# Performance work log

Hardware: AMD Instinct MI355X
Metric: run time of the kernel (lower is better)

Reference implementation:

```python
import jax, jax.numpy as jnp
import numpy as np

EPS = 1e-5  # GroupNorm eps


def setup_inputs() -> dict:
    key = jax.random.key(0)
    ks = jax.random.split(key, 12)
    D, H, I = 512, 8, 64
    B, L = 2, 1024
    g = 0.01  # xavier gain used in reset_parameters
    inp = {
        "x": jax.random.normal(ks[0], (B, L, D), jnp.float32),
        "w_z": jax.random.normal(ks[1], (D, D), jnp.float32) * g,
        "b_z": jnp.zeros((D,), jnp.float32),
        "w_za": jax.random.normal(ks[2], (D, D), jnp.float32) * g,
        "b_za": jnp.zeros((D,), jnp.float32),
        "w_ang": jax.random.normal(ks[3], (D, H), jnp.float32) * g,
        "b_ang": jnp.zeros((H,), jnp.float32),
        "w_abs": jax.random.normal(ks[4], (D, H), jnp.float32) * g,
        "b_abs": jnp.zeros((H,), jnp.float32),
        "w_y": jax.random.normal(ks[5], (D, D), jnp.float32) * g,
        "b_y": jnp.zeros((D,), jnp.float32),
        "w_ya": jax.random.normal(ks[6], (D, D), jnp.float32) * g,
        "b_ya": jnp.zeros((D,), jnp.float32),
        "gn_w": jnp.ones((H,), jnp.float32),
        "gn_b": jnp.zeros((H,), jnp.float32),
        "lc_r": jax.random.normal(ks[7], (H, I), jnp.float32),
        "lc_i": jax.random.normal(ks[8], (H, I), jnp.float32),
    }
    return inp


def reference(x, w_z, b_z, w_za, b_za, w_ang, b_ang, w_abs, b_abs,
              w_y, b_y, w_ya, b_ya, gn_w, gn_b, lc_r, lc_i):
    B, L, D = x.shape
    H = gn_w.shape[0]
    I = D // H
    silu = jax.nn.silu
    xf = x.astype(jnp.float32)

    # gated value, promoted to complex:  [B, L, H, I]
    z = ((xf @ w_z + b_z) * silu(xf @ w_za + b_za)).astype(jnp.complex64).reshape(B, L, H, I)

    # per-head log-decay phazor: [B, L, H] complex
    scale = (0.001 ** jnp.linspace(0.0, 1.0, H)).astype(jnp.float32)
    ln_ph = (silu(xf @ w_ang + b_ang) * 1j - jax.nn.sigmoid(xf @ w_abs + b_abs)) * scale

    # FFT of ones => circular conv with ones = cumulative sum along axis 1
    ones_fft = jnp.fft.fft(jnp.ones((L,), jnp.float32), n=2 * L)

    # ln_phazor repeated over m then tril(-1) over the LAST TWO dims (m, h),
    # exactly matching torch.Tensor.tril semantics on a 'b l m h' tensor.
    masked = jnp.tril(jnp.broadcast_to(ln_ph[:, :, None, :], (B, L, L, H)), -1)
    mfft = jnp.fft.fft(masked, n=2 * L, axis=1)
    mconv = jnp.fft.ifft(mfft * ones_fft[None, :, None, None], axis=1)[:, :L]
    ph_masked = jnp.tril(jnp.exp(mconv))  # tril over (m, h)

    h_inner = jnp.einsum('blmh,bmhi->blhi', ph_masked, z)

    pfft = jnp.fft.fft(ln_ph, n=2 * L, axis=1)
    pconv = jnp.fft.ifft(pfft * ones_fft[None, :, None], axis=1)[:, :L]
    last_conv = lc_r + 1j * lc_i  # [H, I] complex (last_conv_init broadcast over batch)
    h_cross = jnp.exp(pconv)[..., None] * last_conv[None, None]  # [B, L, H, I]

    h = (h_inner + h_cross).real  # [B, L, H, I]

    # GroupNorm(H groups, H channels) on (B*L, H, I): per-(sample, head) norm over I
    mean = h.mean(axis=-1, keepdims=True)
    var = h.var(axis=-1, keepdims=True)
    hn = (h - mean) / jnp.sqrt(var + EPS) * gn_w[:, None] + gn_b[:, None]
    h_norm = hn.reshape(B, L, D)

    y = (h_norm @ w_y + b_y) * silu(xf @ w_ya + b_ya)
    return y.astype(x.dtype)
```

## Files before the change

kernel.cpp:

```cpp
#include <hip/hip_runtime.h>
#include <math.h>

#define D_ 512
#define H_ 8
#define I_ 64
#define L_ 1024

typedef __attribute__((ext_vector_type(8))) short short8;
typedef __attribute__((ext_vector_type(4))) float f32x4;

__device__ __forceinline__ float sigmoidf_(float x) { return 1.f / (1.f + expf(-x)); }
__device__ __forceinline__ float siluf_(float x) { return x / (1.f + expf(-x)); }

__device__ __forceinline__ unsigned short f2bf(float f) {
    unsigned u = __float_as_uint(f);
    u += 0x7fffu + ((u >> 16) & 1u);
    return (unsigned short)(u >> 16);
}
__device__ __forceinline__ float bf2f(unsigned short v) {
    return __uint_as_float((unsigned)v << 16);
}

__global__ __launch_bounds__(256) void k1_prep(
    const float* __restrict__ x, unsigned short* __restrict__ xb, int nconv,
    const float* __restrict__ w0, const float* __restrict__ w1,
    const float* __restrict__ w2, const float* __restrict__ w3,
    unsigned short* __restrict__ t0, unsigned short* __restrict__ t1,
    unsigned short* __restrict__ t2, unsigned short* __restrict__ t3,
    const float* __restrict__ w_ang, const float* __restrict__ b_ang,
    const float* __restrict__ w_abs, const float* __restrict__ b_abs,
    float* __restrict__ a_out, float* __restrict__ r_out)
{
    __shared__ float sm[64][65];
    const int tid = threadIdx.x;
    const int bid = blockIdx.x;
    if (bid < nconv) {
        int gid = bid * 256 + tid;
        float4 v = ((const float4*)x)[gid];
        ushort4 o = { f2bf(v.x), f2bf(v.y), f2bf(v.z), f2bf(v.w) };
        ((ushort4*)xb)[gid] = o;
        return;
    }
    if (bid < nconv + 256) {
        int t = bid - nconv;
        int zsel = t >> 6, tile = t & 63;
        const float* src = zsel == 0 ? w0 : zsel == 1 ? w1 : zsel == 2 ? w2 : w3;
        unsigned short* dst = zsel == 0 ? t0 : zsel == 1 ? t1 : zsel == 2 ? t2 : t3;
        const int k0 = (tile >> 3) * 64, n0 = (tile & 7) * 64;
#pragma unroll
        for (int i = 0; i < 16; ++i) {
            int idx = tid + i * 256;
            int rr = idx >> 6, cc = idx & 63;
            sm[rr][cc] = src[(size_t)(k0 + rr) * 512 + n0 + cc];
        }
        __syncthreads();
#pragma unroll
        for (int i = 0; i < 16; ++i) {
            int idx = tid + i * 256;
            int rr = idx >> 6, cc = idx & 63;
            dst[(size_t)(n0 + rr) * 512 + k0 + cc] = f2bf(sm[cc][rr]);
        }
        return;
    }
    {
        int t = bid - nconv - 256;
        const int s = tid & 3, c = (tid >> 2) & 15, r = tid >> 6;
        const int n = t * 4 + r;
        const int h = c & 7;
        const float* wp = (c < 8) ? w_ang : w_abs;
        const float* xr = x + (size_t)n * D_;
        float acc = 0.f;
#pragma unroll 4
        for (int i = 0; i < 128; ++i) {
            int k = i * 4 + s;
            acc = fmaf(xr[k], wp[k * H_ + h], acc);
        }
        acc += __shfl_xor(acc, 1);
        acc += __shfl_xor(acc, 2);
        if (s == 0) {
            const float scale = expf(-6.9077552789821368f * (h * (1.0f / 7.0f)));
            if (c < 8) { float p = acc + b_ang[h]; a_out[(size_t)n * H_ + h] = siluf_(p) * scale; }
            else       { float p = acc + b_abs[h]; r_out[(size_t)n * H_ + h] = sigmoidf_(p) * scale; }
        }
    }
}

__global__ __launch_bounds__(256) void k2_gemm3_scan(
    const unsigned short* __restrict__ Axb,
    const unsigned short* __restrict__ Wz, const unsigned short* __restrict__ Wza,
    const unsigned short* __restrict__ Wya,
    const float* __restrict__ b_z, const float* __restrict__ b_za, const float* __restrict__ b_ya,
    unsigned short* __restrict__ gateb, float* __restrict__ Zs_part, float* __restrict__ zdiag,
    const float* __restrict__ a_arr, const float* __restrict__ r_arr,
    float* __restrict__ Si, float* __restrict__ Sr, int nby)
{
    __shared__ short As[64 * 32];
    __shared__ short Bs[3][64 * 32];
    __shared__ float red[64][8];
    __shared__ float2 buf[2][256];
    const int tid = threadIdx.x;

    if ((int)blockIdx.y >= nby) {
        const int u = ((int)blockIdx.y - nby) * 8 + (int)blockIdx.x;
        const int b = u >> 3, h = u & 7;
        float2 v[4];
        float2 run = make_float2(0.f, 0.f);
        const size_t base = ((size_t)b * L_ + tid * 4) * H_ + h;
#pragma unroll
        for (int j = 0; j < 4; ++j) {
            run.x += a_arr[base + j * H_];
            run.y += r_arr[base + j * H_];
            v[j] = run;
        }
        buf[0][tid] = run;
        __syncthreads();
        int src = 0;
        for (int off = 1; off < 256; off <<= 1) {
            float2 val = buf[src][tid];
            if (tid >= off) { float2 p = buf[src][tid - off]; val.x += p.x; val.y += p.y; }
            buf[src ^ 1][tid] = val;
            src ^= 1;
            __syncthreads();
        }
        float2 excl = make_float2(0.f, 0.f);
        if (tid > 0) excl = buf[src][tid - 1];
#pragma unroll
        for (int j = 0; j < 4; ++j) {
            Si[base + j * H_] = v[j].x + excl.x;
            Sr[base + j * H_] = -(v[j].y + excl.y);
        }
        return;
    }

    const int lane = tid & 63, w = tid >> 6;
    const int wm = w >> 1, wn = w & 1;
    const int bx = blockIdx.x;
    const int row0 = blockIdx.y * 64, col0 = bx * 64;

    const f32x4 zf = {0.f, 0.f, 0.f, 0.f};
    f32x4 accz[2][2], accza[2][2], accya[2][2];
#pragma unroll
    for (int a = 0; a < 2; ++a)
#pragma unroll
        for (int bq = 0; bq < 2; ++bq) { accz[a][bq] = zf; accza[a][bq] = zf; accya[a][bq] = zf; }

    const int sr = tid >> 2, sc = tid & 3;
    const int sld = sr * 64 + ((sc ^ ((sr >> 1) & 3)) << 4);
    const size_t gA = (size_t)(row0 + sr) * 512 + sc * 8;
    const size_t gB = (size_t)(col0 + sr) * 512 + sc * 8;

    for (int k0 = 0; k0 < 512; k0 += 32) {
        *(int4*)((char*)As + sld)    = *(const int4*)(Axb + gA + k0);
        *(int4*)((char*)Bs[0] + sld) = *(const int4*)(Wz  + gB + k0);
        *(int4*)((char*)Bs[1] + sld) = *(const int4*)(Wza + gB + k0);
        *(int4*)((char*)Bs[2] + sld) = *(const int4*)(Wya + gB + k0);
        __syncthreads();
        short8 af[2], bz[2], bza[2], bya[2];
#pragma unroll
        for (int fi = 0; fi < 2; ++fi) {
            int rr = wm * 32 + fi * 16 + (lane & 15);
            int off = rr * 64 + ((((lane >> 4)) ^ ((rr >> 1) & 3)) << 4);
            af[fi] = *(const short8*)((const char*)As + off);
        }
#pragma unroll
        for (int fj = 0; fj < 2; ++fj) {
            int rr = wn * 32 + fj * 16 + (lane & 15);
            int off = rr * 64 + ((((lane >> 4)) ^ ((rr >> 1) & 3)) << 4);
            bz[fj]  = *(const short8*)((const char*)Bs[0] + off);
            bza[fj] = *(const short8*)((const char*)Bs[1] + off);
            bya[fj] = *(const short8*)((const char*)Bs[2] + off);
        }
#pragma unroll
        for (int fi = 0; fi < 2; ++fi)
#pragma unroll
            for (int fj = 0; fj < 2; ++fj) {
                accz[fi][fj]  = __builtin_amdgcn_mfma_f32_16x16x32_bf16(af[fi], bz[fj],  accz[fi][fj],  0, 0, 0);
                accza[fi][fj] = __builtin_amdgcn_mfma_f32_16x16x32_bf16(af[fi], bza[fj], accza[fi][fj], 0, 0, 0);
                accya[fi][fj] = __builtin_amdgcn_mfma_f32_16x16x32_bf16(af[fi], bya[fj], accya[fi][fj], 0, 0, 0);
            }
        __syncthreads();
    }

    const bool first = (row0 & (L_ - 1)) == 0;
    const int b8 = (row0 >> 10) * 8;
#pragma unroll
    for (int fj = 0; fj < 2; ++fj) {
        float lsum = 0.f;
        int lc = wn * 32 + fj * 16 + (lane & 15);
        int col = col0 + lc;
        float Bz = b_z[col], Bza = b_za[col], Bya = b_ya[col];
#pragma unroll
        for (int fi = 0; fi < 2; ++fi) {
#pragma unroll
            for (int q = 0; q < 4; ++q) {
                int lr = wm * 32 + fi * 16 + ((lane >> 4) << 2) + q;
                int row = row0 + lr;
                float pz = accz[fi][fj][q] + Bz;
                float pza = accza[fi][fj][q] + Bza;
                float v = pz * siluf_(pza);
                gateb[(size_t)row * 512 + col] = f2bf(siluf_(accya[fi][fj][q] + Bya));
                if (!first || lr > bx) lsum += v;
                if (first && lr == bx) zdiag[(b8 + bx) * 64 + lc] = v;
            }
        }
        red[lc][wm * 4 + (lane >> 4)] = lsum;
    }
    __syncthreads();
    if (tid < 64) {
        float s = 0.f;
#pragma unroll
        for (int j = 0; j < 8; ++j) s += red[tid][j];
        Zs_part[((size_t)blockIdx.y * 8 + bx) * 64 + tid] = s;
    }
}

__global__ __launch_bounds__(512) void k3_hgn_gemm_y(
    const unsigned short* __restrict__ Wy, const float* __restrict__ b_y,
    const unsigned short* __restrict__ gateb,
    const float* __restrict__ Sr, const float* __restrict__ Si,
    const float* __restrict__ Zs_part, const float* __restrict__ zdiag,
    const float* __restrict__ lc_r, const float* __restrict__ lc_i,
    const float* __restrict__ gn_w, const float* __restrict__ gn_b,
    float* __restrict__ y)
{
    __shared__ unsigned short hA[64][520];
    __shared__ short Bs[64 * 32];
    __shared__ float Cr[8][65], Ci[8][65], Zd[8][65];
    const int tid = threadIdx.x;
    const int row0 = blockIdx.y * 64, col0 = blockIdx.x * 64;
    const int b = row0 >> 10;

    {
        int h = tid >> 6, i = tid & 63;
        float s = 0.f;
#pragma unroll
        for (int rb = 0; rb < 16; ++rb)
            s += Zs_part[(((size_t)b * 16 + rb) * 8 + h) * 64 + i];
        Cr[h][i] = s + lc_r[h * 64 + i];
        Ci[h][i] = lc_i[h * 64 + i];
        Zd[h][i] = zdiag[((size_t)b * 8 + h) * 64 + i];
    }
    __syncthreads();

    {
        const int r = tid >> 3, h = tid & 7;
        const int row = row0 + r;
        const float sr = Sr[(size_t)row * 8 + h];
        const float si = Si[(size_t)row * 8 + h];
        const float er = expf(sr);
        const float ca = er * cosf(si), sb = er * sinf(si);
        float sum = 0.f, sq = 0.f;
#pragma unroll 8
        for (int i = 0; i < 64; ++i) {
            float hv = Zd[h][i] + ca * Cr[h][i] - sb * Ci[h][i];
            sum += hv; sq += hv * hv;
        }
        const float mean = sum * (1.f / 64.f);
        const float inv = rsqrtf(sq * (1.f / 64.f) - mean * mean + 1e-5f);
        const float gw = gn_w[h] * inv;
        const float gb = gn_b[h] - mean * gw;
#pragma unroll
        for (int s8 = 0; s8 < 8; ++s8) {
            short8 pk;
#pragma unroll
            for (int j = 0; j < 8; ++j) {
                int i = s8 * 8 + j;
                float hv = Zd[h][i] + ca * Cr[h][i] - sb * Ci[h][i];
                pk[j] = (short)f2bf(hv * gw + gb);
            }
            int slot = (s8 + h) & 7;
            *(short8*)((char*)&hA[r][0] + h * 128 + slot * 16) = pk;
        }
    }
    __syncthreads();

    const int lane = tid & 63, w = tid >> 6;
    const int wm = w >> 2, wn = w & 3;
    const f32x4 zf = {0.f, 0.f, 0.f, 0.f};
    f32x4 acc[2] = {zf, zf};

    const int brow = tid >> 3, bsc = tid & 7;
    const size_t gB = (size_t)(col0 + brow) * 512 + bsc * 4;
    const int bwr = brow * 64 + (((bsc >> 1) ^ ((brow >> 1) & 3)) << 4) + (bsc & 1) * 8;

    for (int k0 = 0; k0 < 512; k0 += 32) {
        *(int2*)((char*)Bs + bwr) = *(const int2*)(Wy + gB + k0);
        __syncthreads();
        short8 af[2], bf;
        const int hk = k0 >> 6;
        const int t = ((k0 & 32) >> 3) + (lane >> 4);
        const int slot = (t + hk) & 7;
#pragma unroll
        for (int fi = 0; fi < 2; ++fi) {
            int rr = wm * 32 + fi * 16 + (lane & 15);
            af[fi] = *(const short8*)((const char*)&hA[rr][0] + hk * 128 + slot * 16);
        }
        {
            int rr = wn * 16 + (lane & 15);
            bf = *(const short8*)((const char*)Bs + rr * 64 + (((lane >> 4) ^ ((rr >> 1) & 3)) << 4));
        }
        acc[0] = __builtin_amdgcn_mfma_f32_16x16x32_bf16(af[0], bf, acc[0], 0, 0, 0);
        acc[1] = __builtin_amdgcn_mfma_f32_16x16x32_bf16(af[1], bf, acc[1], 0, 0, 0);
        __syncthreads();
    }

    const int col = col0 + wn * 16 + (lane & 15);
    const float By = b_y[col];
#pragma unroll
    for (int fi = 0; fi < 2; ++fi)
#pragma unroll
        for (int q = 0; q < 4; ++q) {
            int row = row0 + wm * 32 + fi * 16 + ((lane >> 4) << 2) + q;
            size_t idx = (size_t)row * 512 + col;
            y[idx] = (acc[fi][q] + By) * bf2f(gateb[idx]);
        }
}

extern "C" void kernel_launch(void* const* d_in, const int* in_sizes, int n_in,
                              void* d_out, int out_size, void* d_ws, size_t ws_size,
                              hipStream_t stream) {
    (void)n_in; (void)out_size; (void)ws_size;
    const float* x     = (const float*)d_in[0];
    const float* w_z   = (const float*)d_in[1];
    const float* b_z   = (const float*)d_in[2];
    const float* w_za  = (const float*)d_in[3];
    const float* b_za  = (const float*)d_in[4];
    const float* w_ang = (const float*)d_in[5];
    const float* b_ang = (const float*)d_in[6];
    const float* w_abs = (const float*)d_in[7];
    const float* b_abs = (const float*)d_in[8];
    const float* w_y   = (const float*)d_in[9];
    const float* b_y   = (const float*)d_in[10];
    const float* w_ya  = (const float*)d_in[11];
    const float* b_ya  = (const float*)d_in[12];
    const float* gn_w  = (const float*)d_in[13];
    const float* gn_b  = (const float*)d_in[14];
    const float* lc_r  = (const float*)d_in[15];
    const float* lc_i  = (const float*)d_in[16];
    float* y = (float*)d_out;

    const int BL = in_sizes[0] / D_;
    const int B  = BL / L_;

    unsigned short* xb   = (unsigned short*)d_ws;
    unsigned short* wtz  = xb   + (size_t)BL * 512;
    unsigned short* wtza = wtz  + 512 * 512;
    unsigned short* wtya = wtza + 512 * 512;
    unsigned short* wty  = wtya + 512 * 512;
    unsigned short* gateb= wty  + 512 * 512;
    float* a_arr = (float*)(gateb + (size_t)BL * 512);
    float* r_arr = a_arr + (size_t)BL * H_;
    float* Si    = r_arr + (size_t)BL * H_;
    float* Sr    = Si    + (size_t)BL * H_;
    float* zdiag = Sr    + (size_t)BL * H_;
    float* Zs_part = zdiag + (size_t)B * H_ * I_;

    const int nconv = (BL * 512) / 1024;
    const int nby = BL / 64;

    k1_prep<<<nconv + 256 + BL / 4, 256, 0, stream>>>(
        x, xb, nconv, w_z, w_za, w_ya, w_y, wtz, wtza, wtya, wty,
        w_ang, b_ang, w_abs, b_abs, a_arr, r_arr);
    k2_gemm3_scan<<<dim3(8, nby + 2), 256, 0, stream>>>(
        xb, wtz, wtza, wtya, b_z, b_za, b_ya,
        gateb, Zs_part, zdiag, a_arr, r_arr, Si, Sr, nby);
    k3_hgn_gemm_y<<<dim3(8, nby), 512, 0, stream>>>(
        wty, b_y, gateb, Sr, Si, Zs_part, zdiag, lc_r, lc_i, gn_w, gn_b, y);
}
```

Baseline: 47.24 us.

## Double-buffer GEMM tiles via global_load_lds and fuse decay projections into scan blocks

```diff
diff --git a/kernel.cpp b/kernel.cpp
--- a/kernel.cpp
+++ b/kernel.cpp
@@ -19,6 +19,11 @@
 }
 __device__ __forceinline__ float bf2f(unsigned short v) {
     return __uint_as_float((unsigned)v << 16);
+}
+
+__device__ __forceinline__ void load_lds16(const void* g, void* l) {
+    __builtin_amdgcn_global_load_lds((const __attribute__((address_space(1))) void*)g,
+                                     (__attribute__((address_space(3))) void*)l, 16, 0, 0);
 }
 
 __global__ __launch_bounds__(256) void k1_prep(
@@ -27,9 +32,8 @@
     const float* __restrict__ w2, const float* __restrict__ w3,
     unsigned short* __restrict__ t0, unsigned short* __restrict__ t1,
     unsigned short* __restrict__ t2, unsigned short* __restrict__ t3,
-    const float* __restrict__ w_ang, const float* __restrict__ b_ang,
-    const float* __restrict__ w_abs, const float* __restrict__ b_abs,
-    float* __restrict__ a_out, float* __restrict__ r_out)
+    const float* __restrict__ w_ang, const float* __restrict__ w_abs,
+    float* __restrict__ wat, float* __restrict__ wrt)
 {
     __shared__ float sm[64][65];
     const int tid = threadIdx.x;
@@ -63,24 +67,10 @@
         return;
     }
     {
-        int t = bid - nconv - 256;
-        const int s = tid & 3, c = (tid >> 2) & 15, r = tid >> 6;
-        const int n = t * 4 + r;
-        const int h = c & 7;
-        const float* wp = (c < 8) ? w_ang : w_abs;
-        const float* xr = x + (size_t)n * D_;
-        float acc = 0.f;
-#pragma unroll 4
-        for (int i = 0; i < 128; ++i) {
-            int k = i * 4 + s;
-            acc = fmaf(xr[k], wp[k * H_ + h], acc);
-        }
-        acc += __shfl_xor(acc, 1);
-        acc += __shfl_xor(acc, 2);
-        if (s == 0) {
-            const float scale = expf(-6.9077552789821368f * (h * (1.0f / 7.0f)));
-            if (c < 8) { float p = acc + b_ang[h]; a_out[(size_t)n * H_ + h] = siluf_(p) * scale; }
-            else       { float p = acc + b_abs[h]; r_out[(size_t)n * H_ + h] = sigmoidf_(p) * scale; }
+        int h = bid - nconv - 256;
+        for (int k = tid; k < 512; k += 256) {
+            wat[h * 512 + k] = w_ang[k * 8 + h];
+            wrt[h * 512 + k] = w_abs[k * 8 + h];
         }
     }
 }
@@ -91,25 +81,39 @@
     const unsigned short* __restrict__ Wya,
     const float* __restrict__ b_z, const float* __restrict__ b_za, const float* __restrict__ b_ya,
     unsigned short* __restrict__ gateb, float* __restrict__ Zs_part, float* __restrict__ zdiag,
-    const float* __restrict__ a_arr, const float* __restrict__ r_arr,
-    float* __restrict__ Si, float* __restrict__ Sr, int nby)
+    const float* __restrict__ x, const float* __restrict__ wat, const float* __restrict__ wrt,
+    const float* __restrict__ b_ang, const float* __restrict__ b_abs,
+    float* __restrict__ Si, float* __restrict__ Sr)
 {
-    __shared__ short As[64 * 32];
-    __shared__ short Bs[3][64 * 32];
+    __shared__ short As[2][2048];
+    __shared__ short Bs[2][3][2048];
     __shared__ float red[64][8];
     __shared__ float2 buf[2][256];
     const int tid = threadIdx.x;
 
-    if ((int)blockIdx.y >= nby) {
-        const int u = ((int)blockIdx.y - nby) * 8 + (int)blockIdx.x;
-        const int b = u >> 3, h = u & 7;
+    if ((int)blockIdx.y < 2) {
+        const int b = blockIdx.y, h = blockIdx.x;
+        const float scale = expf(-6.9077552789821368f * (h * (1.0f / 7.0f)));
+        const float ba = b_ang[h], br = b_abs[h];
+        const float4* wa4 = (const float4*)(wat + h * 512);
+        const float4* wr4 = (const float4*)(wrt + h * 512);
         float2 v[4];
         float2 run = make_float2(0.f, 0.f);
-        const size_t base = ((size_t)b * L_ + tid * 4) * H_ + h;
+        const float* xp = x + ((size_t)b * L_ + tid * 4) * 512;
 #pragma unroll
         for (int j = 0; j < 4; ++j) {
-            run.x += a_arr[base + j * H_];
-            run.y += r_arr[base + j * H_];
+            const float4* xr = (const float4*)(xp + (size_t)j * 512);
+            float aA = 0.f, aR = 0.f;
+#pragma unroll 8
+            for (int q = 0; q < 128; ++q) {
+                float4 xv = xr[q], wa = wa4[q], wr = wr4[q];
+                aA = fmaf(xv.x, wa.x, aA); aA = fmaf(xv.y, wa.y, aA);
+                aA = fmaf(xv.z, wa.z, aA); aA = fmaf(xv.w, wa.w, aA);
+                aR = fmaf(xv.x, wr.x, aR); aR = fmaf(xv.y, wr.y, aR);
+                aR = fmaf(xv.z, wr.z, aR); aR = fmaf(xv.w, wr.w, aR);
+            }
+            run.x += siluf_(aA + ba) * scale;
+            run.y += sigmoidf_(aR + br) * scale;
             v[j] = run;
         }
         buf[0][tid] = run;
@@ -124,6 +128,7 @@
         }
         float2 excl = make_float2(0.f, 0.f);
         if (tid > 0) excl = buf[src][tid - 1];
+        const size_t base = ((size_t)b * L_ + tid * 4) * H_ + h;
 #pragma unroll
         for (int j = 0; j < 4; ++j) {
             Si[base + j * H_] = v[j].x + excl.x;
@@ -135,7 +140,8 @@
     const int lane = tid & 63, w = tid >> 6;
     const int wm = w >> 1, wn = w & 1;
     const int bx = blockIdx.x;
-    const int row0 = blockIdx.y * 64, col0 = bx * 64;
+    const int rblk = (int)blockIdx.y - 2;
+    const int row0 = rblk * 64, col0 = bx * 64;
 
     const f32x4 zf = {0.f, 0.f, 0.f, 0.f};
     f32x4 accz[2][2], accza[2][2], accya[2][2];
@@ -144,31 +150,41 @@
 #pragma unroll
         for (int bq = 0; bq < 2; ++bq) { accz[a][bq] = zf; accza[a][bq] = zf; accya[a][bq] = zf; }
 
-    const int sr = tid >> 2, sc = tid & 3;
-    const int sld = sr * 64 + ((sc ^ ((sr >> 1) & 3)) << 4);
-    const size_t gA = (size_t)(row0 + sr) * 512 + sc * 8;
-    const size_t gB = (size_t)(col0 + sr) * 512 + sc * 8;
-
-    for (int k0 = 0; k0 < 512; k0 += 32) {
-        *(int4*)((char*)As + sld)    = *(const int4*)(Axb + gA + k0);
-        *(int4*)((char*)Bs[0] + sld) = *(const int4*)(Wz  + gB + k0);
-        *(int4*)((char*)Bs[1] + sld) = *(const int4*)(Wza + gB + k0);
-        *(int4*)((char*)Bs[2] + sld) = *(const int4*)(Wya + gB + k0);
-        __syncthreads();
+    const int ssr = w * 16 + (lane >> 2);
+    const int ssc = (lane & 3) ^ ((ssr >> 1) & 3);
+    const size_t gA = (size_t)(row0 + ssr) * 512 + ssc * 8;
+    const size_t gB = (size_t)(col0 + ssr) * 512 + ssc * 8;
+    const int ldso = w * 1024;
+
+    load_lds16(Axb + gA, (char*)As[0] + ldso);
+    load_lds16(Wz  + gB, (char*)Bs[0][0] + ldso);
+    load_lds16(Wza + gB, (char*)Bs[0][1] + ldso);
+    load_lds16(Wya + gB, (char*)Bs[0][2] + ldso);
+    __syncthreads();
+
+    int cur = 0;
+    for (int s = 0; s < 16; ++s) {
+        if (s < 15) {
+            const int k1 = (s + 1) * 32;
+            load_lds16(Axb + gA + k1, (char*)As[cur ^ 1] + ldso);
+            load_lds16(Wz  + gB + k1, (char*)Bs[cur ^ 1][0] + ldso);
+            load_lds16(Wza + gB + k1, (char*)Bs[cur ^ 1][1] + ldso);
+            load_lds16(Wya + gB + k1, (char*)Bs[cur ^ 1][2] + ldso);
+        }
         short8 af[2], bz[2], bza[2], bya[2];
 #pragma unroll
         for (int fi = 0; fi < 2; ++fi) {
             int rr = wm * 32 + fi * 16 + (lane & 15);
             int off = rr * 64 + ((((lane >> 4)) ^ ((rr >> 1) & 3)) << 4);
-            af[fi] = *(const short8*)((const char*)As + off);
+            af[fi] = *(const short8*)((const char*)As[cur] + off);
         }
 #pragma unroll
         for (int fj = 0; fj < 2; ++fj) {
             int rr = wn * 32 + fj * 16 + (lane & 15);
             int off = rr * 64 + ((((lane >> 4)) ^ ((rr >> 1) & 3)) << 4);
-            bz[fj]  = *(const short8*)((const char*)Bs[0] + off);
-            bza[fj] = *(const short8*)((const char*)Bs[1] + off);
-            bya[fj] = *(const short8*)((const char*)Bs[2] + off);
+            bz[fj]  = *(const short8*)((const char*)Bs[cur][0] + off);
+            bza[fj] = *(const short8*)((const char*)Bs[cur][1] + off);
+            bya[fj] = *(const short8*)((const char*)Bs[cur][2] + off);
         }
 #pragma unroll
         for (int fi = 0; fi < 2; ++fi)
@@ -179,10 +195,11 @@
                 accya[fi][fj] = __builtin_amdgcn_mfma_f32_16x16x32_bf16(af[fi], bya[fj], accya[fi][fj], 0, 0, 0);
             }
         __syncthreads();
-    }
-
-    const bool first = (row0 & (L_ - 1)) == 0;
-    const int b8 = (row0 >> 10) * 8;
+        cur ^= 1;
+    }
+
+    const bool first = (rblk & 15) == 0;
+    const int b8 = (rblk >> 4) * 8;
 #pragma unroll
     for (int fj = 0; fj < 2; ++fj) {
         float lsum = 0.f;
@@ -210,7 +227,7 @@
         float s = 0.f;
 #pragma unroll
         for (int j = 0; j < 8; ++j) s += red[tid][j];
-        Zs_part[((size_t)blockIdx.y * 8 + bx) * 64 + tid] = s;
+        Zs_part[((size_t)rblk * 8 + bx) * 64 + tid] = s;
     }
 }
 
@@ -224,11 +241,20 @@
     float* __restrict__ y)
 {
     __shared__ unsigned short hA[64][520];
-    __shared__ short Bs[64 * 32];
+    __shared__ short Bs[2][2048];
     __shared__ float Cr[8][65], Ci[8][65], Zd[8][65];
     const int tid = threadIdx.x;
+    const int lane = tid & 63, w = tid >> 6;
     const int row0 = blockIdx.y * 64, col0 = blockIdx.x * 64;
     const int b = row0 >> 10;
+
+    size_t gB = 0;
+    if (w < 4) {
+        const int ssr = w * 16 + (lane >> 2);
+        const int ssc = (lane & 3) ^ ((ssr >> 1) & 3);
+        gB = (size_t)(col0 + ssr) * 512 + ssc * 8;
+        load_lds16(Wy + gB, (char*)Bs[0] + w * 1024);
+    }
 
     {
         int h = tid >> 6, i = tid & 63;
@@ -274,18 +300,15 @@
     }
     __syncthreads();
 
-    const int lane = tid & 63, w = tid >> 6;
     const int wm = w >> 2, wn = w & 3;
     const f32x4 zf = {0.f, 0.f, 0.f, 0.f};
     f32x4 acc[2] = {zf, zf};
 
-    const int brow = tid >> 3, bsc = tid & 7;
-    const size_t gB = (size_t)(col0 + brow) * 512 + bsc * 4;
-    const int bwr = brow * 64 + (((bsc >> 1) ^ ((brow >> 1) & 3)) << 4) + (bsc & 1) * 8;
-
-    for (int k0 = 0; k0 < 512; k0 += 32) {
-        *(int2*)((char*)Bs + bwr) = *(const int2*)(Wy + gB + k0);
-        __syncthreads();
+    int cur = 0;
+    for (int s = 0; s < 16; ++s) {
+        if (s < 15 && w < 4)
+            load_lds16(Wy + gB + (s + 1) * 32, (char*)Bs[cur ^ 1] + w * 1024);
+        const int k0 = s * 32;
         short8 af[2], bf;
         const int hk = k0 >> 6;
         const int t = ((k0 & 32) >> 3) + (lane >> 4);
@@ -297,11 +320,12 @@
         }
         {
             int rr = wn * 16 + (lane & 15);
-            bf = *(const short8*)((const char*)Bs + rr * 64 + (((lane >> 4) ^ ((rr >> 1) & 3)) << 4));
+            bf = *(const short8*)((const char*)Bs[cur] + rr * 64 + (((lane >> 4) ^ ((rr >> 1) & 3)) << 4));
         }
         acc[0] = __builtin_amdgcn_mfma_f32_16x16x32_bf16(af[0], bf, acc[0], 0, 0, 0);
         acc[1] = __builtin_amdgcn_mfma_f32_16x16x32_bf16(af[1], bf, acc[1], 0, 0, 0);
         __syncthreads();
+        cur ^= 1;
     }
 
     const int col = col0 + wn * 16 + (lane & 15);
@@ -348,22 +372,22 @@
     unsigned short* wtya = wtza + 512 * 512;
     unsigned short* wty  = wtya + 512 * 512;
     unsigned short* gateb= wty  + 512 * 512;
-    float* a_arr = (float*)(gateb + (size_t)BL * 512);
-    float* r_arr = a_arr + (size_t)BL * H_;
-    float* Si    = r_arr + (size_t)BL * H_;
+    float* Si    = (float*)(gateb + (size_t)BL * 512);
     float* Sr    = Si    + (size_t)BL * H_;
     float* zdiag = Sr    + (size_t)BL * H_;
     float* Zs_part = zdiag + (size_t)B * H_ * I_;
+    float* wat   = Zs_part + (size_t)(BL / 64) * H_ * I_;
+    float* wrt   = wat + 8 * 512;
 
     const int nconv = (BL * 512) / 1024;
     const int nby = BL / 64;
 
-    k1_prep<<<nconv + 256 + BL / 4, 256, 0, stream>>>(
+    k1_prep<<<nconv + 256 + 8, 256, 0, stream>>>(
         x, xb, nconv, w_z, w_za, w_ya, w_y, wtz, wtza, wtya, wty,
-        w_ang, b_ang, w_abs, b_abs, a_arr, r_arr);
+        w_ang, w_abs, wat, wrt);
     k2_gemm3_scan<<<dim3(8, nby + 2), 256, 0, stream>>>(
         xb, wtz, wtza, wtya, b_z, b_za, b_ya,
-        gateb, Zs_part, zdiag, a_arr, r_arr, Si, Sr, nby);
+        gateb, Zs_part, zdiag, x, wat, wrt, b_ang, b_abs, Si, Sr);
     k3_hgn_gemm_y<<<dim3(8, nby), 512, 0, stream>>>(
         wty, b_y, gateb, Sr, Si, Zs_part, zdiag, lc_r, lc_i, gn_w, gn_b, y);
 }
```

New measurement: 86.96 us. 84.1% more time.

## Fuse x bf16 conversion into GEMM load and double-buffer LDS in both GEMMs

Applied to the files above, without the earlier changes.

```diff
diff --git a/kernel.cpp b/kernel.cpp
--- a/kernel.cpp
+++ b/kernel.cpp
@@ -22,7 +22,7 @@
 }
 
 __global__ __launch_bounds__(256) void k1_prep(
-    const float* __restrict__ x, unsigned short* __restrict__ xb, int nconv,
+    const float* __restrict__ x,
     const float* __restrict__ w0, const float* __restrict__ w1,
     const float* __restrict__ w2, const float* __restrict__ w3,
     unsigned short* __restrict__ t0, unsigned short* __restrict__ t1,
@@ -34,16 +34,8 @@
     __shared__ float sm[64][65];
     const int tid = threadIdx.x;
     const int bid = blockIdx.x;
-    if (bid < nconv) {
-        int gid = bid * 256 + tid;
-        float4 v = ((const float4*)x)[gid];
-        ushort4 o = { f2bf(v.x), f2bf(v.y), f2bf(v.z), f2bf(v.w) };
-        ((ushort4*)xb)[gid] = o;
-        return;
-    }
-    if (bid < nconv + 256) {
-        int t = bid - nconv;
-        int zsel = t >> 6, tile = t & 63;
+    if (bid < 256) {
+        int zsel = bid >> 6, tile = bid & 63;
         const float* src = zsel == 0 ? w0 : zsel == 1 ? w1 : zsel == 2 ? w2 : w3;
         unsigned short* dst = zsel == 0 ? t0 : zsel == 1 ? t1 : zsel == 2 ? t2 : t3;
         const int k0 = (tile >> 3) * 64, n0 = (tile & 7) * 64;
@@ -63,7 +55,7 @@
         return;
     }
     {
-        int t = bid - nconv - 256;
+        int t = bid - 256;
         const int s = tid & 3, c = (tid >> 2) & 15, r = tid >> 6;
         const int n = t * 4 + r;
         const int h = c & 7;
@@ -86,23 +78,22 @@
 }
 
 __global__ __launch_bounds__(256) void k2_gemm3_scan(
-    const unsigned short* __restrict__ Axb,
+    const float* __restrict__ x,
     const unsigned short* __restrict__ Wz, const unsigned short* __restrict__ Wza,
     const unsigned short* __restrict__ Wya,
     const float* __restrict__ b_z, const float* __restrict__ b_za, const float* __restrict__ b_ya,
     unsigned short* __restrict__ gateb, float* __restrict__ Zs_part, float* __restrict__ zdiag,
     const float* __restrict__ a_arr, const float* __restrict__ r_arr,
-    float* __restrict__ Si, float* __restrict__ Sr, int nby)
+    float* __restrict__ Si, float* __restrict__ Sr)
 {
-    __shared__ short As[64 * 32];
-    __shared__ short Bs[3][64 * 32];
+    __shared__ short As[2][2048];
+    __shared__ short Bs[2][3][2048];
     __shared__ float red[64][8];
     __shared__ float2 buf[2][256];
     const int tid = threadIdx.x;
 
-    if ((int)blockIdx.y >= nby) {
-        const int u = ((int)blockIdx.y - nby) * 8 + (int)blockIdx.x;
-        const int b = u >> 3, h = u & 7;
+    if ((int)blockIdx.y < 2) {
+        const int b = blockIdx.y, h = blockIdx.x;
         float2 v[4];
         float2 run = make_float2(0.f, 0.f);
         const size_t base = ((size_t)b * L_ + tid * 4) * H_ + h;
@@ -135,7 +126,8 @@
     const int lane = tid & 63, w = tid >> 6;
     const int wm = w >> 1, wn = w & 1;
     const int bx = blockIdx.x;
-    const int row0 = blockIdx.y * 64, col0 = bx * 64;
+    const int rblk = (int)blockIdx.y - 2;
+    const int row0 = rblk * 64, col0 = bx * 64;
 
     const f32x4 zf = {0.f, 0.f, 0.f, 0.f};
     f32x4 accz[2][2], accza[2][2], accya[2][2];
@@ -146,29 +138,50 @@
 
     const int sr = tid >> 2, sc = tid & 3;
     const int sld = sr * 64 + ((sc ^ ((sr >> 1) & 3)) << 4);
-    const size_t gA = (size_t)(row0 + sr) * 512 + sc * 8;
-    const size_t gB = (size_t)(col0 + sr) * 512 + sc * 8;
-
-    for (int k0 = 0; k0 < 512; k0 += 32) {
-        *(int4*)((char*)As + sld)    = *(const int4*)(Axb + gA + k0);
-        *(int4*)((char*)Bs[0] + sld) = *(const int4*)(Wz  + gB + k0);
-        *(int4*)((char*)Bs[1] + sld) = *(const int4*)(Wza + gB + k0);
-        *(int4*)((char*)Bs[2] + sld) = *(const int4*)(Wya + gB + k0);
-        __syncthreads();
+    const float* gAx = x + (size_t)(row0 + sr) * 512 + sc * 8;
+    const unsigned short* gWz  = Wz  + (size_t)(col0 + sr) * 512 + sc * 8;
+    const unsigned short* gWza = Wza + (size_t)(col0 + sr) * 512 + sc * 8;
+    const unsigned short* gWya = Wya + (size_t)(col0 + sr) * 512 + sc * 8;
+
+    float4 ra0, ra1; int4 rz, rza, rya;
+#define K2_LOAD(K) { ra0 = *(const float4*)(gAx + (K)); ra1 = *(const float4*)(gAx + (K) + 4); \
+                     rz  = *(const int4*)(gWz  + (K)); rza = *(const int4*)(gWza + (K)); \
+                     rya = *(const int4*)(gWya + (K)); }
+#define K2_WRITE(BUF) { short8 ab; \
+                        ab[0]=(short)f2bf(ra0.x); ab[1]=(short)f2bf(ra0.y); \
+                        ab[2]=(short)f2bf(ra0.z); ab[3]=(short)f2bf(ra0.w); \
+                        ab[4]=(short)f2bf(ra1.x); ab[5]=(short)f2bf(ra1.y); \
+                        ab[6]=(short)f2bf(ra1.z); ab[7]=(short)f2bf(ra1.w); \
+                        *(short8*)((char*)As[BUF] + sld) = ab; \
+                        *(int4*)((char*)Bs[BUF][0] + sld) = rz; \
+                        *(int4*)((char*)Bs[BUF][1] + sld) = rza; \
+                        *(int4*)((char*)Bs[BUF][2] + sld) = rya; }
+
+    K2_LOAD(0);
+    K2_WRITE(0);
+    K2_LOAD(32);
+    __syncthreads();
+
+    int cur = 0;
+    for (int s = 0; s < 16; ++s) {
+        if (s < 15) {
+            K2_WRITE(cur ^ 1);
+            if (s < 14) K2_LOAD((s + 2) * 32);
+        }
         short8 af[2], bz[2], bza[2], bya[2];
 #pragma unroll
         for (int fi = 0; fi < 2; ++fi) {
             int rr = wm * 32 + fi * 16 + (lane & 15);
             int off = rr * 64 + ((((lane >> 4)) ^ ((rr >> 1) & 3)) << 4);
-            af[fi] = *(const short8*)((const char*)As + off);
+            af[fi] = *(const short8*)((const char*)As[cur] + off);
         }
 #pragma unroll
         for (int fj = 0; fj < 2; ++fj) {
             int rr = wn * 32 + fj * 16 + (lane & 15);
             int off = rr * 64 + ((((lane >> 4)) ^ ((rr >> 1) & 3)) << 4);
-            bz[fj]  = *(const short8*)((const char*)Bs[0] + off);
-            bza[fj] = *(const short8*)((const char*)Bs[1] + off);
-            bya[fj] = *(const short8*)((const char*)Bs[2] + off);
+            bz[fj]  = *(const short8*)((const char*)Bs[cur][0] + off);
+            bza[fj] = *(const short8*)((const char*)Bs[cur][1] + off);
+            bya[fj] = *(const short8*)((const char*)Bs[cur][2] + off);
         }
 #pragma unroll
         for (int fi = 0; fi < 2; ++fi)
@@ -179,10 +192,11 @@
                 accya[fi][fj] = __builtin_amdgcn_mfma_f32_16x16x32_bf16(af[fi], bya[fj], accya[fi][fj], 0, 0, 0);
             }
         __syncthreads();
-    }
-
-    const bool first = (row0 & (L_ - 1)) == 0;
-    const int b8 = (row0 >> 10) * 8;
+        cur ^= 1;
+    }
+
+    const bool first = (rblk & 15) == 0;
+    const int b8 = (rblk >> 4) * 8;
 #pragma unroll
     for (int fj = 0; fj < 2; ++fj) {
         float lsum = 0.f;
@@ -210,7 +224,7 @@
         float s = 0.f;
 #pragma unroll
         for (int j = 0; j < 8; ++j) s += red[tid][j];
-        Zs_part[((size_t)blockIdx.y * 8 + bx) * 64 + tid] = s;
+        Zs_part[((size_t)rblk * 8 + bx) * 64 + tid] = s;
     }
 }
 
@@ -224,11 +238,18 @@
     float* __restrict__ y)
 {
     __shared__ unsigned short hA[64][520];
-    __shared__ short Bs[64 * 32];
+    __shared__ short Bs[2][2048];
     __shared__ float Cr[8][65], Ci[8][65], Zd[8][65];
     const int tid = threadIdx.x;
+    const int lane = tid & 63, w = tid >> 6;
     const int row0 = blockIdx.y * 64, col0 = blockIdx.x * 64;
     const int b = row0 >> 10;
+
+    const int brow = tid >> 3, bsc = tid & 7;
+    const size_t gB = (size_t)(col0 + brow) * 512 + bsc * 4;
+    const int bwr = brow * 64 + (((bsc >> 1) ^ ((brow >> 1) & 3)) << 4) + (bsc & 1) * 8;
+    int2 rw0 = *(const int2*)(Wy + gB);
+    int2 rw1 = *(const int2*)(Wy + gB + 32);
 
     {
         int h = tid >> 6, i = tid & 63;
@@ -272,20 +293,20 @@
             *(short8*)((char*)&hA[r][0] + h * 128 + slot * 16) = pk;
         }
     }
+    *(int2*)((char*)Bs[0] + bwr) = rw0;
     __syncthreads();
 
-    const int lane = tid & 63, w = tid >> 6;
     const int wm = w >> 2, wn = w & 3;
     const f32x4 zf = {0.f, 0.f, 0.f, 0.f};
     f32x4 acc[2] = {zf, zf};
 
-    const int brow = tid >> 3, bsc = tid & 7;
-    const size_t gB = (size_t)(col0 + brow) * 512 + bsc * 4;
-    const int bwr = brow * 64 + (((bsc >> 1) ^ ((brow >> 1) & 3)) << 4) + (bsc & 1) * 8;
-
-    for (int k0 = 0; k0 < 512; k0 += 32) {
-        *(int2*)((char*)Bs + bwr) = *(const int2*)(Wy + gB + k0);
-        __syncthreads();
+    int cur = 0;
+    for (int s = 0; s < 16; ++s) {
+        if (s < 15) {
+            *(int2*)((char*)Bs[cur ^ 1] + bwr) = rw1;
+            if (s < 14) rw1 = *(const int2*)(Wy + gB + (s + 2) * 32);
+        }
+        const int k0 = s * 32;
         short8 af[2], bf;
         const int hk = k0 >> 6;
         const int t = ((k0 & 32) >> 3) + (lane >> 4);
@@ -297,11 +318,12 @@
         }
         {
             int rr = wn * 16 + (lane & 15);
-            bf = *(const short8*)((const char*)Bs + rr * 64 + (((lane >> 4) ^ ((rr >> 1) & 3)) << 4));
+            bf = *(const short8*)((const char*)Bs[cur] + rr * 64 + (((lane >> 4) ^ ((rr >> 1) & 3)) << 4));
         }
         acc[0] = __builtin_amdgcn_mfma_f32_16x16x32_bf16(af[0], bf, acc[0], 0, 0, 0);
         acc[1] = __builtin_amdgcn_mfma_f32_16x16x32_bf16(af[1], bf, acc[1], 0, 0, 0);
         __syncthreads();
+        cur ^= 1;
     }
 
     const int col = col0 + wn * 16 + (lane & 15);
@@ -342,8 +364,7 @@
     const int BL = in_sizes[0] / D_;
     const int B  = BL / L_;
 
-    unsigned short* xb   = (unsigned short*)d_ws;
-    unsigned short* wtz  = xb   + (size_t)BL * 512;
+    unsigned short* wtz  = (unsigned short*)d_ws;
     unsigned short* wtza = wtz  + 512 * 512;
     unsigned short* wtya = wtza + 512 * 512;
     unsigned short* wty  = wtya + 512 * 512;
@@ -355,15 +376,14 @@
     float* zdiag = Sr    + (size_t)BL * H_;
     float* Zs_part = zdiag + (size_t)B * H_ * I_;
 
-    const int nconv = (BL * 512) / 1024;
     const int nby = BL / 64;
 
-    k1_prep<<<nconv + 256 + BL / 4, 256, 0, stream>>>(
-        x, xb, nconv, w_z, w_za, w_ya, w_y, wtz, wtza, wtya, wty,
+    k1_prep<<<256 + BL / 4, 256, 0, stream>>>(
+        x, w_z, w_za, w_ya, w_y, wtz, wtza, wtya, wty,
         w_ang, b_ang, w_abs, b_abs, a_arr, r_arr);
     k2_gemm3_scan<<<dim3(8, nby + 2), 256, 0, stream>>>(
-        xb, wtz, wtza, wtya, b_z, b_za, b_ya,
-        gateb, Zs_part, zdiag, a_arr, r_arr, Si, Sr, nby);
+        x, wtz, wtza, wtya, b_z, b_za, b_ya,
+        gateb, Zs_part, zdiag, a_arr, r_arr, Si, Sr);
     k3_hgn_gemm_y<<<dim3(8, nby), 512, 0, stream>>>(
         wty, b_y, gateb, Sr, Si, Zs_part, zdiag, lc_r, lc_i, gn_w, gn_b, y);
 }
```

Measured after the change: 46.07 us. 2.5% less time.
